# Kernel optimization log

Measured on AMD Instinct MI355X. Metric: run time of the kernel, lower is better.

Reference implementation:

```python
import jax, jax.numpy as jnp
import numpy as np

B, T, C, H = 4, 4096, 1024, 64

def setup_inputs() -> dict:
    key = jax.random.key(0)
    kx, kk, kq, kv = jax.random.split(key, 4)
    x = jax.random.normal(kx, (B, T, C), dtype=jnp.float32)
    Wk = jax.random.normal(kk, (C, H), dtype=jnp.float32) * (C ** -0.5)
    Wq = jax.random.normal(kq, (C, H), dtype=jnp.float32) * (C ** -0.5)
    Wv = jax.random.normal(kv, (C, H), dtype=jnp.float32) * (C ** -0.5)
    return {"x": x, "Wk": Wk, "Wq": Wq, "Wv": Wv}

def reference(x, Wk, Wq, Wv):
    Bb, Tt, Cc = x.shape
    k = jnp.einsum('btc,ch->bth', x, Wk)
    q = jnp.einsum('btc,ch->bth', x, Wq)
    v = jnp.einsum('btc,ch->bth', x, Wv)
    # NOTE: source scales by C**-0.5 with C = embed dim (not head_size)
    scores = jnp.einsum('bqh,bkh->bqk', q, k) * (Cc ** -0.5)
    causal = jnp.tril(jnp.ones((Tt, Tt), dtype=bool))
    scores = jnp.where(causal, scores, -jnp.inf)
    weights = jax.nn.softmax(scores, axis=-1)
    out = jnp.einsum('bqk,bkh->bqh', weights, v)
    return out
```

## Files before the change

### kernel.cpp

```cpp
#include <hip/hip_runtime.h>
#include <hip/hip_bf16.h>

typedef _Float16 f16x8 __attribute__((ext_vector_type(8)));
typedef _Float16 f16x4 __attribute__((ext_vector_type(4)));
typedef __fp16 fp16x2 __attribute__((ext_vector_type(2)));
typedef float f32x4 __attribute__((ext_vector_type(4)));

#define BATCH 4
#define SEQ 4096
#define EMB 1024
#define HEAD 64

__device__ __forceinline__ void async_copy16(const void* gsrc, void* ldst) {
  __builtin_amdgcn_global_load_lds(
      (const __attribute__((address_space(1))) void*)gsrc,
      (__attribute__((address_space(3))) void*)ldst,
      16, 0, 0);
}

__global__ __launch_bounds__(256) void wtrans_kernel(
    const float* __restrict__ Wk, const float* __restrict__ Wq,
    const float* __restrict__ Wv, _Float16* __restrict__ WT) {
  int id = blockIdx.x * 256 + threadIdx.x;
  int step = id / 1536;
  int rem = id - step * 1536;
  int G = rem / 192;
  int n = rem - G * 192;
  int sel = n >> 6;
  int col = n & 63;
  const float* src = (sel == 0) ? Wq : (sel == 1) ? Wk : Wv;
  const float scale = (sel == 0) ? 0.03125f : 1.0f;
  f16x8 u;
#pragma unroll
  for (int j = 0; j < 8; ++j) {
    int k = step * 64 + G * 8 + j;
    u[j] = (_Float16)(src[k * 64 + col] * scale);
  }
  *(f16x8*)(WT + (size_t)id * 8) = u;
}

__global__ __launch_bounds__(256) void proj_kernel(
    const float* __restrict__ x, const _Float16* __restrict__ WT,
    _Float16* __restrict__ Qh, _Float16* __restrict__ KT,
    _Float16* __restrict__ VT) {
  __shared__ _Float16 wtl[2][12288];
  __shared__ float xls[3][32 * 64];
  const int tid = threadIdx.x;
  const int wave = tid >> 6;
  const int lane = tid & 63;
  const int quad = lane >> 4;
  const int l16 = lane & 15;
  const int wm = wave & 1;
  const int wn = wave >> 1;
  const int rowblk = blockIdx.x * 32;

  const int lq = lane >> 4;
  const int pos = lane & 15;

  f32x4 acc[6];
#pragma unroll
  for (int t = 0; t < 6; ++t) acc[t] = (f32x4){0.f, 0.f, 0.f, 0.f};

#pragma unroll
  for (int i = 0; i < 6; ++i) {
    const int c = wave * 6 + i;
    async_copy16(WT + (size_t)c * 512 + lane * 8, (char*)&wtl[0][0] + c * 1024);
  }
#pragma unroll
  for (int i = 0; i < 2; ++i) {
    const int c = wave * 2 + i;
    const int rts = c * 4 + lq;
    const int u = pos ^ (rts & 7);
    async_copy16(x + (size_t)(rowblk + rts) * EMB + u * 4,
                 (char*)&xls[0][0] + c * 1024);
  }
#pragma unroll
  for (int i = 0; i < 2; ++i) {
    const int c = wave * 2 + i;
    const int rts = c * 4 + lq;
    const int u = pos ^ (rts & 7);
    async_copy16(x + (size_t)(rowblk + rts) * EMB + 64 + u * 4,
                 (char*)&xls[1][0] + c * 1024);
  }

  const int rt = wm * 16 + l16;
  const int rb = rt & 7;
  const int ua = ((quad * 2) ^ rb) * 4;
  const int ub = ((quad * 2 + 1) ^ rb) * 4;
  const int uc = ((8 + quad * 2) ^ rb) * 4;
  const int ud = ((8 + quad * 2 + 1) ^ rb) * 4;

  int pw = 0;
  int x3 = 0;
  int x3i = 2;
  for (int step = 0; step < 16; ++step) {
    if (step < 15) {
      asm volatile("s_waitcnt vmcnt(2)" ::: "memory");
    } else {
      asm volatile("s_waitcnt vmcnt(0)" ::: "memory");
    }
    __builtin_amdgcn_sched_barrier(0);
    __builtin_amdgcn_s_barrier();

    if (step + 1 < 16) {
      const _Float16* wsrc = WT + (size_t)(step + 1) * 12288;
#pragma unroll
      for (int i = 0; i < 6; ++i) {
        const int c = wave * 6 + i;
        async_copy16(wsrc + (size_t)c * 512 + lane * 8,
                     (char*)&wtl[pw ^ 1][0] + c * 1024);
      }
    }
    if (step + 2 < 16) {
      const float* xsrc = x + (size_t)(step + 2) * 64;
#pragma unroll
      for (int i = 0; i < 2; ++i) {
        const int c = wave * 2 + i;
        const int rts = c * 4 + lq;
        const int u = pos ^ (rts & 7);
        async_copy16(xsrc + (size_t)(rowblk + rts) * EMB + u * 4,
                     (char*)&xls[x3i][0] + c * 1024);
      }
    }

    const float* xl = &xls[x3][rt * 64];
    const float4 xa = *(const float4*)(xl + ua);
    const float4 xb = *(const float4*)(xl + ub);
    const float4 xc = *(const float4*)(xl + uc);
    const float4 xd = *(const float4*)(xl + ud);
    fp16x2 p0 = __builtin_amdgcn_cvt_pkrtz(xa.x, xa.y);
    fp16x2 p1 = __builtin_amdgcn_cvt_pkrtz(xa.z, xa.w);
    fp16x2 p2 = __builtin_amdgcn_cvt_pkrtz(xb.x, xb.y);
    fp16x2 p3 = __builtin_amdgcn_cvt_pkrtz(xb.z, xb.w);
    f16x8 af0, af1;
    af0[0] = (_Float16)p0[0]; af0[1] = (_Float16)p0[1];
    af0[2] = (_Float16)p1[0]; af0[3] = (_Float16)p1[1];
    af0[4] = (_Float16)p2[0]; af0[5] = (_Float16)p2[1];
    af0[6] = (_Float16)p3[0]; af0[7] = (_Float16)p3[1];
    p0 = __builtin_amdgcn_cvt_pkrtz(xc.x, xc.y);
    p1 = __builtin_amdgcn_cvt_pkrtz(xc.z, xc.w);
    p2 = __builtin_amdgcn_cvt_pkrtz(xd.x, xd.y);
    p3 = __builtin_amdgcn_cvt_pkrtz(xd.z, xd.w);
    af1[0] = (_Float16)p0[0]; af1[1] = (_Float16)p0[1];
    af1[2] = (_Float16)p1[0]; af1[3] = (_Float16)p1[1];
    af1[4] = (_Float16)p2[0]; af1[5] = (_Float16)p2[1];
    af1[6] = (_Float16)p3[0]; af1[7] = (_Float16)p3[1];
#pragma unroll
    for (int t = 0; t < 6; ++t) {
      const int n = wn * 96 + t * 16 + l16;
      const f16x8 b0 = *(const f16x8*)&wtl[pw][(size_t)((0 * 4 + quad) * 192 + n) * 8];
      const f16x8 b1 = *(const f16x8*)&wtl[pw][(size_t)((1 * 4 + quad) * 192 + n) * 8];
      acc[t] = __builtin_amdgcn_mfma_f32_16x16x32_f16(af0, b0, acc[t], 0, 0, 0);
      acc[t] = __builtin_amdgcn_mfma_f32_16x16x32_f16(af1, b1, acc[t], 0, 0, 0);
    }
    pw ^= 1;
    x3 = (x3 == 2) ? 0 : x3 + 1;
    x3i = (x3i == 2) ? 0 : x3i + 1;
  }

  const int rowbase = rowblk + wm * 16;
  const int b = rowbase >> 12;
  const int trbase = (rowbase & 4095) + quad * 4;
#pragma unroll
  for (int t = 0; t < 6; ++t) {
    const int g = wn * 6 + t;
    if (g < 4) {
      const int h = g * 16 + l16;
#pragma unroll
      for (int r = 0; r < 4; ++r)
        Qh[(size_t)(rowbase + quad * 4 + r) * HEAD + h] = (_Float16)acc[t][r];
    } else if (g < 8) {
      const int h = (g - 4) * 16 + l16;
#pragma unroll
      for (int r = 0; r < 4; ++r) {
        const int t0 = trbase + r;
        const size_t ad = ((size_t)((b * 64 + (t0 >> 6)) * 8 + (h >> 3)) * 64 +
                           (t0 & 63)) * 8 + (h & 7);
        KT[ad] = (_Float16)acc[t][r];
      }
    } else {
      const int h = (g - 8) * 16 + l16;
      f16x4 pk;
      pk[0] = (_Float16)acc[t][0]; pk[1] = (_Float16)acc[t][1];
      pk[2] = (_Float16)acc[t][2]; pk[3] = (_Float16)acc[t][3];
      const size_t ad = ((size_t)((b * 64 + (trbase >> 6)) * 8 + ((trbase & 63) >> 3)) * 512) +
                        (size_t)h * 8 + (trbase & 7);
      *(f16x4*)(VT + ad) = pk;
    }
  }
}

__global__ __launch_bounds__(512) void flash_kernel(
    const _Float16* __restrict__ Qh, const _Float16* __restrict__ KT,
    const _Float16* __restrict__ VT, float* __restrict__ out) {
  __shared__ _Float16 myp[8][32 * 68];
  __shared__ float lds_o[2][4][32][68];
  __shared__ float lds_l[2][4][32];
  const int tid = threadIdx.x;
  const int w = tid >> 6;
  const int lane = tid & 63;
  const int quad = lane >> 4;
  const int l16 = lane & 15;
  const int b = blockIdx.x & 3;
  const int jj = blockIdx.x >> 2;
  const int t = w >> 2;
  const int q = w & 3;
  const int j = t ? (127 - jj) : jj;
  const int qb = j * 32;
  const int nkt = (j >> 1) + 1;
  const int lo = (nkt * q) >> 2;
  const int hi = (nkt * (q + 1)) >> 2;

  const _Float16* Q = Qh + (size_t)b * SEQ * HEAD;
  const _Float16* KTb = KT + (size_t)b * 64 * 4096;
  const _Float16* VTb = VT + (size_t)b * 64 * 4096;
  const f32x4 zero = {0.f, 0.f, 0.f, 0.f};
  _Float16* mp = &myp[w][0];

  f16x8 aq0[2], aq1[2];
#pragma unroll
  for (int rt = 0; rt < 2; ++rt) {
    aq0[rt] = *(const f16x8*)(Q + (size_t)(qb + rt * 16 + l16) * HEAD + quad * 8);
    aq1[rt] = *(const f16x8*)(Q + (size_t)(qb + rt * 16 + l16) * HEAD + 32 + quad * 8);
  }

  f32x4 oc[2][4];
#pragma unroll
  for (int rt = 0; rt < 2; ++rt)
#pragma unroll
    for (int m = 0; m < 4; ++m) oc[rt][m] = zero;
  float lacc[2][4] = {{0.f, 0.f, 0.f, 0.f}, {0.f, 0.f, 0.f, 0.f}};

  f16x8 ka[4], kb[4];
  if (lo < hi) {
    const _Float16* kp = KTb + (size_t)lo * 4096;
#pragma unroll
    for (int s = 0; s < 4; ++s) {
      ka[s] = *(const f16x8*)(kp + (size_t)quad * 512 + (s * 16 + l16) * 8);
      kb[s] = *(const f16x8*)(kp + (size_t)(4 + quad) * 512 + (s * 16 + l16) * 8);
    }
  }

  for (int kt = lo; kt < hi; ++kt) {
    const _Float16* vp = VTb + (size_t)kt * 4096;
    f16x8 va[4], vb[4];
#pragma unroll
    for (int m = 0; m < 4; ++m) {
      va[m] = *(const f16x8*)(vp + (size_t)quad * 512 + (m * 16 + l16) * 8);
      vb[m] = *(const f16x8*)(vp + (size_t)(4 + quad) * 512 + (m * 16 + l16) * 8);
    }

    f32x4 sc[2][4];
#pragma unroll
    for (int s = 0; s < 4; ++s) {
#pragma unroll
      for (int rt = 0; rt < 2; ++rt) {
        sc[rt][s] = __builtin_amdgcn_mfma_f32_16x16x32_f16(aq0[rt], ka[s], zero, 0, 0, 0);
        sc[rt][s] = __builtin_amdgcn_mfma_f32_16x16x32_f16(aq1[rt], kb[s], sc[rt][s], 0, 0, 0);
      }
    }

    if (kt + 1 < hi) {
      const _Float16* kp = KTb + (size_t)(kt + 1) * 4096;
#pragma unroll
      for (int s = 0; s < 4; ++s) {
        ka[s] = *(const f16x8*)(kp + (size_t)quad * 512 + (s * 16 + l16) * 8);
        kb[s] = *(const f16x8*)(kp + (size_t)(4 + quad) * 512 + (s * 16 + l16) * 8);
      }
    }

    const int kbase = kt * 64;
    if (kt == nkt - 1) {
#pragma unroll
      for (int rt = 0; rt < 2; ++rt) {
        const int qrow = qb + rt * 16 + quad * 4;
#pragma unroll
        for (int s = 0; s < 4; ++s) {
#pragma unroll
          for (int r = 0; r < 4; ++r) {
            const float pv = (kbase + s * 16 + l16 > qrow + r) ? 0.f : __expf(sc[rt][s][r]);
            lacc[rt][r] += pv;
            mp[(rt * 16 + quad * 4 + r) * 68 + s * 16 + l16] = (_Float16)pv;
          }
        }
      }
    } else {
#pragma unroll
      for (int rt = 0; rt < 2; ++rt) {
#pragma unroll
        for (int s = 0; s < 4; ++s) {
#pragma unroll
          for (int r = 0; r < 4; ++r) {
            const float pv = __expf(sc[rt][s][r]);
            lacc[rt][r] += pv;
            mp[(rt * 16 + quad * 4 + r) * 68 + s * 16 + l16] = (_Float16)pv;
          }
        }
      }
    }

#pragma unroll
    for (int rt = 0; rt < 2; ++rt) {
      const f16x8 ap0 = *(const f16x8*)(mp + (rt * 16 + l16) * 68 + quad * 8);
      const f16x8 ap1 = *(const f16x8*)(mp + (rt * 16 + l16) * 68 + 32 + quad * 8);
#pragma unroll
      for (int m = 0; m < 4; ++m) {
        oc[rt][m] = __builtin_amdgcn_mfma_f32_16x16x32_f16(ap0, va[m], oc[rt][m], 0, 0, 0);
        oc[rt][m] = __builtin_amdgcn_mfma_f32_16x16x32_f16(ap1, vb[m], oc[rt][m], 0, 0, 0);
      }
    }
  }

#pragma unroll
  for (int rt = 0; rt < 2; ++rt) {
#pragma unroll
    for (int r = 0; r < 4; ++r) {
      float l = lacc[rt][r];
      l += __shfl_xor(l, 1);
      l += __shfl_xor(l, 2);
      l += __shfl_xor(l, 4);
      l += __shfl_xor(l, 8);
      const int row = rt * 16 + quad * 4 + r;
      if (l16 == 0) lds_l[t][q][row] = l;
#pragma unroll
      for (int m = 0; m < 4; ++m)
        lds_o[t][q][row][m * 16 + l16] = oc[rt][m][r];
    }
  }
  __syncthreads();

  {
    const int row = q * 8 + (lane >> 3);
    const int h8 = (lane & 7) * 8;
    const int jt = t ? (127 - jj) : jj;
    const float lsum = lds_l[t][0][row] + lds_l[t][1][row] +
                       lds_l[t][2][row] + lds_l[t][3][row];
    const float inv = 1.0f / lsum;
    float4 o0, o1;
#pragma unroll
    for (int i = 0; i < 4; ++i) {
      ((float*)&o0)[i] = (lds_o[t][0][row][h8 + i] + lds_o[t][1][row][h8 + i] +
                          lds_o[t][2][row][h8 + i] + lds_o[t][3][row][h8 + i]) * inv;
      ((float*)&o1)[i] = (lds_o[t][0][row][h8 + 4 + i] + lds_o[t][1][row][h8 + 4 + i] +
                          lds_o[t][2][row][h8 + 4 + i] + lds_o[t][3][row][h8 + 4 + i]) * inv;
    }
    float* op = out + ((size_t)b * SEQ + jt * 32 + row) * HEAD + h8;
    *(float4*)op = o0;
    *(float4*)(op + 4) = o1;
  }
}

extern "C" void kernel_launch(void* const* d_in, const int* in_sizes, int n_in,
                              void* d_out, int out_size, void* d_ws, size_t ws_size,
                              hipStream_t stream) {
  const float* x  = (const float*)d_in[0];
  const float* Wk = (const float*)d_in[1];
  const float* Wq = (const float*)d_in[2];
  const float* Wv = (const float*)d_in[3];
  float* out = (float*)d_out;

  char* ws = (char*)d_ws;
  _Float16* Qh = (_Float16*)(ws);
  _Float16* KT = (_Float16*)(ws + (size_t)2 * 1024 * 1024);
  _Float16* VT = (_Float16*)(ws + (size_t)4 * 1024 * 1024);
  _Float16* WT = (_Float16*)(ws + (size_t)6 * 1024 * 1024);

  wtrans_kernel<<<96, 256, 0, stream>>>(Wk, Wq, Wv, WT);
  proj_kernel<<<512, 256, 0, stream>>>(x, WT, Qh, KT, VT);
  flash_kernel<<<256, 512, 0, stream>>>(Qh, KT, VT, out);
}
```

Baseline: 135.7 us.

## Load projection operands directly into registers, dropping LDS staging and barriers

The projection kernel no longer stages weights and x tiles through shared memory with async copies and block barriers. Each wave loads its weight fragments and x values straight from global memory into registers, prefetching the next K step while the current MFMAs run. The K loop start is rotated per block so different blocks hit different weight slices at the same time. This removes LDS traffic and synchronisation but adds redundant global and L2 reads of the weights across waves, and adds register pressure.

```diff
diff --git a/kernel.cpp b/kernel.cpp
--- a/kernel.cpp
+++ b/kernel.cpp
@@ -43,8 +43,6 @@
     const float* __restrict__ x, const _Float16* __restrict__ WT,
     _Float16* __restrict__ Qh, _Float16* __restrict__ KT,
     _Float16* __restrict__ VT) {
-  __shared__ _Float16 wtl[2][12288];
-  __shared__ float xls[3][32 * 64];
   const int tid = threadIdx.x;
   const int wave = tid >> 6;
   const int lane = tid & 63;
@@ -53,81 +51,30 @@
   const int wm = wave & 1;
   const int wn = wave >> 1;
   const int rowblk = blockIdx.x * 32;
-
-  const int lq = lane >> 4;
-  const int pos = lane & 15;
+  const int koff = blockIdx.x & 15;
+
+  const float* xr = x + (size_t)(rowblk + wm * 16 + l16) * EMB + quad * 8;
+  const int nbase = wn * 96 + l16;
 
   f32x4 acc[6];
 #pragma unroll
   for (int t = 0; t < 6; ++t) acc[t] = (f32x4){0.f, 0.f, 0.f, 0.f};
 
-#pragma unroll
-  for (int i = 0; i < 6; ++i) {
-    const int c = wave * 6 + i;
-    async_copy16(WT + (size_t)c * 512 + lane * 8, (char*)&wtl[0][0] + c * 1024);
-  }
-#pragma unroll
-  for (int i = 0; i < 2; ++i) {
-    const int c = wave * 2 + i;
-    const int rts = c * 4 + lq;
-    const int u = pos ^ (rts & 7);
-    async_copy16(x + (size_t)(rowblk + rts) * EMB + u * 4,
-                 (char*)&xls[0][0] + c * 1024);
-  }
-#pragma unroll
-  for (int i = 0; i < 2; ++i) {
-    const int c = wave * 2 + i;
-    const int rts = c * 4 + lq;
-    const int u = pos ^ (rts & 7);
-    async_copy16(x + (size_t)(rowblk + rts) * EMB + 64 + u * 4,
-                 (char*)&xls[1][0] + c * 1024);
-  }
-
-  const int rt = wm * 16 + l16;
-  const int rb = rt & 7;
-  const int ua = ((quad * 2) ^ rb) * 4;
-  const int ub = ((quad * 2 + 1) ^ rb) * 4;
-  const int uc = ((8 + quad * 2) ^ rb) * 4;
-  const int ud = ((8 + quad * 2 + 1) ^ rb) * 4;
-
-  int pw = 0;
-  int x3 = 0;
-  int x3i = 2;
+  f16x8 wb[12];
+  {
+    const _Float16* wp = WT + ((size_t)koff * 1536 + quad * 192 + nbase) * 8;
+#pragma unroll
+    for (int t = 0; t < 6; ++t) {
+      wb[t * 2]     = *(const f16x8*)(wp + (size_t)t * 128);
+      wb[t * 2 + 1] = *(const f16x8*)(wp + 6144 + (size_t)t * 128);
+    }
+  }
+  float4 xa = *(const float4*)(xr + koff * 64);
+  float4 xb = *(const float4*)(xr + koff * 64 + 4);
+  float4 xc = *(const float4*)(xr + koff * 64 + 32);
+  float4 xd = *(const float4*)(xr + koff * 64 + 36);
+
   for (int step = 0; step < 16; ++step) {
-    if (step < 15) {
-      asm volatile("s_waitcnt vmcnt(2)" ::: "memory");
-    } else {
-      asm volatile("s_waitcnt vmcnt(0)" ::: "memory");
-    }
-    __builtin_amdgcn_sched_barrier(0);
-    __builtin_amdgcn_s_barrier();
-
-    if (step + 1 < 16) {
-      const _Float16* wsrc = WT + (size_t)(step + 1) * 12288;
-#pragma unroll
-      for (int i = 0; i < 6; ++i) {
-        const int c = wave * 6 + i;
-        async_copy16(wsrc + (size_t)c * 512 + lane * 8,
-                     (char*)&wtl[pw ^ 1][0] + c * 1024);
-      }
-    }
-    if (step + 2 < 16) {
-      const float* xsrc = x + (size_t)(step + 2) * 64;
-#pragma unroll
-      for (int i = 0; i < 2; ++i) {
-        const int c = wave * 2 + i;
-        const int rts = c * 4 + lq;
-        const int u = pos ^ (rts & 7);
-        async_copy16(xsrc + (size_t)(rowblk + rts) * EMB + u * 4,
-                     (char*)&xls[x3i][0] + c * 1024);
-      }
-    }
-
-    const float* xl = &xls[x3][rt * 64];
-    const float4 xa = *(const float4*)(xl + ua);
-    const float4 xb = *(const float4*)(xl + ub);
-    const float4 xc = *(const float4*)(xl + uc);
-    const float4 xd = *(const float4*)(xl + ud);
     fp16x2 p0 = __builtin_amdgcn_cvt_pkrtz(xa.x, xa.y);
     fp16x2 p1 = __builtin_amdgcn_cvt_pkrtz(xa.z, xa.w);
     fp16x2 p2 = __builtin_amdgcn_cvt_pkrtz(xb.x, xb.y);
@@ -145,17 +92,31 @@
     af1[2] = (_Float16)p1[0]; af1[3] = (_Float16)p1[1];
     af1[4] = (_Float16)p2[0]; af1[5] = (_Float16)p2[1];
     af1[6] = (_Float16)p3[0]; af1[7] = (_Float16)p3[1];
+
+    if (step < 15) {
+      const int ksn = (step + 1 + koff) & 15;
+      const float* xn = xr + ksn * 64;
+      xa = *(const float4*)(xn);
+      xb = *(const float4*)(xn + 4);
+      xc = *(const float4*)(xn + 32);
+      xd = *(const float4*)(xn + 36);
+    }
+
 #pragma unroll
     for (int t = 0; t < 6; ++t) {
-      const int n = wn * 96 + t * 16 + l16;
-      const f16x8 b0 = *(const f16x8*)&wtl[pw][(size_t)((0 * 4 + quad) * 192 + n) * 8];
-      const f16x8 b1 = *(const f16x8*)&wtl[pw][(size_t)((1 * 4 + quad) * 192 + n) * 8];
-      acc[t] = __builtin_amdgcn_mfma_f32_16x16x32_f16(af0, b0, acc[t], 0, 0, 0);
-      acc[t] = __builtin_amdgcn_mfma_f32_16x16x32_f16(af1, b1, acc[t], 0, 0, 0);
-    }
-    pw ^= 1;
-    x3 = (x3 == 2) ? 0 : x3 + 1;
-    x3i = (x3i == 2) ? 0 : x3i + 1;
+      acc[t] = __builtin_amdgcn_mfma_f32_16x16x32_f16(af0, wb[t * 2], acc[t], 0, 0, 0);
+      acc[t] = __builtin_amdgcn_mfma_f32_16x16x32_f16(af1, wb[t * 2 + 1], acc[t], 0, 0, 0);
+    }
+
+    if (step < 15) {
+      const int ksn = (step + 1 + koff) & 15;
+      const _Float16* wp = WT + ((size_t)ksn * 1536 + quad * 192 + nbase) * 8;
+#pragma unroll
+      for (int t = 0; t < 6; ++t) {
+        wb[t * 2]     = *(const f16x8*)(wp + (size_t)t * 128);
+        wb[t * 2 + 1] = *(const f16x8*)(wp + 6144 + (size_t)t * 128);
+      }
+    }
   }
 
   const int rowbase = rowblk + wm * 16;
```

Measured after the change: 144.0 us. +6.1%, slower.
